# Optimization experiments

Measured on AMD Instinct MI355X. Metric: run time of the kernel, lower is better.

## Reference

```python
import jax, jax.numpy as jnp
import numpy as np

NUM_HEADS = 8
NUM_GROUPS = 32  # min(32, channels=256)
EPS = 1e-5


def group_norm(x, w, b):
    # x: [B, C, L]
    B, C, L = x.shape
    xg = x.reshape(B, NUM_GROUPS, C // NUM_GROUPS, L)
    mu = xg.mean(axis=(2, 3), keepdims=True)
    var = xg.var(axis=(2, 3), keepdims=True)
    xn = ((xg - mu) * jax.lax.rsqrt(var + EPS)).reshape(B, C, L)
    return xn * w[None, :, None] + b[None, :, None]


def setup_inputs() -> dict:
    key = jax.random.key(0)
    ks = jax.random.split(key, 5)
    B, C, L = 4, 256, 2048
    x = jax.random.normal(ks[0], (B, C, L), dtype=jnp.float32)
    gn_w = jnp.ones((C,), dtype=jnp.float32)
    gn_b = jnp.zeros((C,), dtype=jnp.float32)
    qkv_w = jax.random.normal(ks[1], (3 * C, C), dtype=jnp.float32) * (C ** -0.5)
    qkv_b = jax.random.normal(ks[2], (3 * C,), dtype=jnp.float32) * 0.02
    out_w = jax.random.normal(ks[3], (C, C), dtype=jnp.float32) * (C ** -0.5)
    out_b = jax.random.normal(ks[4], (C,), dtype=jnp.float32) * 0.02
    return {"x": x, "gn_w": gn_w, "gn_b": gn_b, "qkv_w": qkv_w,
            "qkv_b": qkv_b, "out_w": out_w, "out_b": out_b}


def reference(x, gn_w, gn_b, qkv_w, qkv_b, out_w, out_b):
    B, C, L = x.shape
    H = NUM_HEADS
    D = C // H
    h = group_norm(x, gn_w, gn_b)
    # 1x1 conv == channel matmul: [B,3C,L]
    qkv = jnp.einsum('oc,bcl->bol', qkv_w, h) + qkv_b[None, :, None]
    qkv = qkv.reshape(B, 3, H, D, L)
    q, k, v = qkv[:, 0], qkv[:, 1], qkv[:, 2]  # each [B,H,D,L]
    scale = D ** -0.5
    attn = jnp.einsum('bhdn,bhdm->bhnm', q * scale, k)  # [B,H,L,L]
    attn = jax.nn.softmax(attn, axis=-1)
    h = jnp.einsum('bhnm,bhdm->bhdn', attn, v).reshape(B, C, L)
    out = jnp.einsum('oc,bcl->bol', out_w, h) + out_b[None, :, None]
    return x + out
```

## Files before the change

### kernel.cpp

```cpp
#include <hip/hip_runtime.h>
#include <math.h>

using f32x4  = __attribute__((ext_vector_type(4))) float;
using bf16x8 = __attribute__((ext_vector_type(8))) short;

constexpr int kB = 4, kC = 256, kL = 2048, kH = 8;
constexpr float kQScale = 0.25505402264f;

__device__ __forceinline__ unsigned short f2bf(float f) {
    unsigned u = __builtin_bit_cast(unsigned, f);
    u += 0x7fffu + ((u >> 16) & 1u);
    return (unsigned short)(u >> 16);
}
__device__ __forceinline__ unsigned cvt_pk(float lo, float hi) {
    unsigned r;
    asm("v_cvt_pk_bf16_f32 %0, %1, %2" : "=v"(r) : "v"(lo), "v"(hi));
    return r;
}
__device__ __forceinline__ f32x4 mfma16(bf16x8 a, bf16x8 b, f32x4 c) {
    return __builtin_amdgcn_mfma_f32_16x16x32_bf16(a, b, c, 0, 0, 0);
}
__device__ __forceinline__ bf16x8 bc8(unsigned a, unsigned b, unsigned c, unsigned d) {
    return __builtin_bit_cast(bf16x8, make_uint4(a, b, c, d));
}
__device__ __forceinline__ void glds16(const unsigned short* g, unsigned short* l) {
    __builtin_amdgcn_global_load_lds(
        (const __attribute__((address_space(1))) unsigned int*)g,
        (__attribute__((address_space(3))) unsigned int*)l, 16, 0, 0);
}

__global__ __launch_bounds__(256) void gncvt_kernel(const float* __restrict__ x,
                                                    const float* __restrict__ gw,
                                                    const float* __restrict__ gb,
                                                    unsigned short* __restrict__ hT,
                                                    const float* __restrict__ qkvw,
                                                    const float* __restrict__ outw,
                                                    unsigned short* __restrict__ wq,
                                                    unsigned short* __restrict__ wo) {
    if (blockIdx.x >= 128) {
        int i = (blockIdx.x - 128) * 256 + threadIdx.x;
        const float* s; unsigned short* d; int j;
        if (i < 49152) { s = qkvw; d = wq; j = i; }
        else           { s = outw; d = wo; j = i - 49152; }
        float4 v = ((const float4*)s)[j];
        ((uint2*)d)[j] = make_uint2(cvt_pk(v.x, v.y), cvt_pk(v.z, v.w));
        return;
    }
    int b = blockIdx.x >> 5, g = blockIdx.x & 31;
    int t = threadIdx.x;
    const float* xp = x + ((size_t)b * kC + g * 8) * kL + 8 * t;

    float v[8][8];
    float s = 0.f, ss = 0.f;
#pragma unroll
    for (int c = 0; c < 8; ++c) {
        float4 a  = *(const float4*)(xp + (size_t)c * kL);
        float4 a2 = *(const float4*)(xp + (size_t)c * kL + 4);
        v[c][0]=a.x; v[c][1]=a.y; v[c][2]=a.z; v[c][3]=a.w;
        v[c][4]=a2.x; v[c][5]=a2.y; v[c][6]=a2.z; v[c][7]=a2.w;
        s  += (a.x+a.y)+(a.z+a.w)+(a2.x+a2.y)+(a2.z+a2.w);
        ss += a.x*a.x+a.y*a.y+a.z*a.z+a.w*a.w+a2.x*a2.x+a2.y*a2.y+a2.z*a2.z+a2.w*a2.w;
    }
#pragma unroll
    for (int off = 32; off; off >>= 1) {
        s  += __shfl_down(s, off);
        ss += __shfl_down(ss, off);
    }
    __shared__ float red[8];
    int wv = t >> 6;
    if ((t & 63) == 0) { red[wv] = s; red[4 + wv] = ss; }
    __syncthreads();
    s  = red[0] + red[1] + red[2] + red[3];
    ss = red[4] + red[5] + red[6] + red[7];
    float mean = s * (1.f / 16384.f);
    float var  = ss * (1.f / 16384.f) - mean * mean;
    float rstd = rsqrtf(var + 1e-5f);

    float wc[8], bc[8];
#pragma unroll
    for (int c = 0; c < 8; ++c) { wc[c] = gw[g*8+c] * rstd; bc[c] = gb[g*8+c]; }

    unsigned short* hp = hT + ((size_t)b * kL + 8 * t) * kC + g * 8;
#pragma unroll
    for (int j = 0; j < 8; ++j) {
        unsigned pk[4];
#pragma unroll
        for (int c2 = 0; c2 < 4; ++c2) {
            pk[c2] = cvt_pk((v[2*c2  ][j] - mean) * wc[2*c2  ] + bc[2*c2  ],
                            (v[2*c2+1][j] - mean) * wc[2*c2+1] + bc[2*c2+1]);
        }
        *(uint4*)(hp + (size_t)j * kC) = make_uint4(pk[0], pk[1], pk[2], pk[3]);
    }
}

__device__ __forceinline__ void store_qk(unsigned short* __restrict__ base, size_t bh,
                                         int n, int d0, f32x4 acc,
                                         const float* bias4, float scale) {
    float v0 = (acc[0] + bias4[0]) * scale, v1 = (acc[1] + bias4[1]) * scale;
    float v2 = (acc[2] + bias4[2]) * scale, v3 = (acc[3] + bias4[3]) * scale;
    *(uint2*)(base + (bh * kL + n) * 32 + d0) = make_uint2(cvt_pk(v0, v1), cvt_pk(v2, v3));
}

__global__ __launch_bounds__(256) void qkv_gemm(const unsigned short* __restrict__ Wb,
                                                const unsigned short* __restrict__ hT,
                                                const float* __restrict__ qkvb,
                                                unsigned short* __restrict__ qT,
                                                unsigned short* __restrict__ kT,
                                                unsigned short* __restrict__ vbuf) {
    __shared__ alignas(16) unsigned short Hlds[2][8][512];
    int t = threadIdx.x, wv = t >> 6, ll = t & 15, lg = (t >> 4) & 3;
    int lane = t & 63;
    int n0 = blockIdx.x * 128, o0 = blockIdx.y * 64, b = blockIdx.z;
    int obase = o0 + wv * 16;
    const unsigned short* hb = hT + (size_t)b * kL * kC;

    bf16x8 wf[8];
#pragma unroll
    for (int k = 0; k < 8; ++k)
        wf[k] = *(const bf16x8*)(Wb + (size_t)(obase + ll) * 256 + 32 * k + 8 * lg);
    float bias[4];
#pragma unroll
    for (int r = 0; r < 4; ++r) bias[r] = qkvb[obase + 4 * lg + r];
    int mode = (obase < 256) ? 0 : (obase < 512 ? 1 : 2);
    int d0 = (obase & 31) + 4 * lg;

    const unsigned short* hsrc0 = hb + (size_t)(n0 + 16 * (2 * wv)     + ll) * 256 + 8 * lg;
    const unsigned short* hsrc1 = hb + (size_t)(n0 + 16 * (2 * wv + 1) + ll) * 256 + 8 * lg;

    glds16(hsrc0,      &Hlds[0][2 * wv][0]);
    glds16(hsrc1,      &Hlds[0][2 * wv + 1][0]);
    glds16(hsrc0 + 32, &Hlds[1][2 * wv][0]);
    glds16(hsrc1 + 32, &Hlds[1][2 * wv + 1][0]);
    asm volatile("s_waitcnt vmcnt(2)" ::: "memory");
    __builtin_amdgcn_sched_barrier(0);
    __builtin_amdgcn_s_barrier();

    f32x4 acc[8] = {};
    int cur = 0;
    for (int c = 0; c < 8; ++c) {
        bf16x8 hf[8];
#pragma unroll
        for (int nj = 0; nj < 8; ++nj)
            hf[nj] = *(const bf16x8*)&Hlds[cur][nj][lane * 8];
        asm volatile("s_waitcnt lgkmcnt(0)" ::: "memory");
        __builtin_amdgcn_sched_barrier(0);
        __builtin_amdgcn_s_barrier();

        int kn = ((c + 2) & 7) * 32;
        glds16(hsrc0 + kn, &Hlds[cur][2 * wv][0]);
        glds16(hsrc1 + kn, &Hlds[cur][2 * wv + 1][0]);

        __builtin_amdgcn_s_setprio(1);
#pragma unroll
        for (int nj = 0; nj < 8; ++nj)
            acc[nj] = mfma16(wf[c], hf[nj], acc[nj]);
        __builtin_amdgcn_s_setprio(0);

        asm volatile("s_waitcnt vmcnt(2)" ::: "memory");
        __builtin_amdgcn_sched_barrier(0);
        __builtin_amdgcn_s_barrier();
        cur ^= 1;
    }
    asm volatile("s_waitcnt vmcnt(0)" ::: "memory");

#pragma unroll
    for (int nj = 0; nj < 8; ++nj) {
        int n = n0 + 16 * nj + ll;
        if (mode == 0) {
            store_qk(qT, (size_t)b * kH + (obase >> 5), n, d0, acc[nj], bias, kQScale);
        } else if (mode == 1) {
            store_qk(kT, (size_t)b * kH + ((obase - 256) >> 5), n, d0, acc[nj], bias, 1.f);
        } else {
#pragma unroll
            for (int r = 0; r < 4; ++r) {
                size_t row = (size_t)b * kC + (obase - 512) + 4 * lg + r;
                vbuf[row * kL + n] = f2bf(acc[nj][r] + bias[r]);
            }
        }
    }
}

__global__ __launch_bounds__(256) void attn_kernel(const unsigned short* __restrict__ qT,
                                                   const unsigned short* __restrict__ kT,
                                                   const unsigned short* __restrict__ vbuf,
                                                   unsigned short* __restrict__ h2T) {
    __shared__ alignas(16) unsigned short Klds[2][4][512];
    __shared__ alignas(16) unsigned short Vlds[2][4][512];
    __shared__ unsigned Plds[4][16][34];
    int t = threadIdx.x, wv = t >> 6, ll = t & 15, hi = (t >> 4) & 3;
    int lane = t & 63;
    int j = blockIdx.x;
    int bid = (j & 7) * 128 + (j >> 3);
    int qg = bid & 31, bh = bid >> 5;
    int b = bh >> 3, h = bh & 7;
    const unsigned short* qb = qT + (size_t)bh * kL * 32;
    const unsigned short* kb = kT + (size_t)bh * kL * 32;
    const unsigned short* vb = vbuf + ((size_t)b * kC + h * 32) * kL;
    int nq = qg * 64 + wv * 16;

    bf16x8 qf = *(const bf16x8*)(qb + (size_t)(nq + ll) * 32 + 8 * hi);

    f32x4 acc[2] = {};
    float lsum = 0.f;
    const f32x4 zero = {0.f, 0.f, 0.f, 0.f};

    const unsigned short* ksrc = kb + (size_t)(16 * wv + ll) * 32 + 8 * hi;
    const unsigned short* vsrc = vb + (size_t)(16 * (wv >> 1) + ll) * kL + 32 * (wv & 1) + 8 * hi;

    glds16(ksrc, &Klds[0][wv][0]);
    glds16(vsrc, &Vlds[0][wv][0]);
    glds16(ksrc + (size_t)64 * 32, &Klds[1][wv][0]);
    glds16(vsrc + 64,              &Vlds[1][wv][0]);
    asm volatile("s_waitcnt vmcnt(2)" ::: "memory");
    __builtin_amdgcn_sched_barrier(0);
    __builtin_amdgcn_s_barrier();

    int cur = 0;
    for (int it = 0; it < 32; ++it) {
        bf16x8 ka[4], va[2][2];
#pragma unroll
        for (int mj = 0; mj < 4; ++mj)
            ka[mj] = *(const bf16x8*)&Klds[cur][mj][lane * 8];
#pragma unroll
        for (int dj = 0; dj < 2; ++dj)
#pragma unroll
            for (int tt = 0; tt < 2; ++tt)
                va[dj][tt] = *(const bf16x8*)&Vlds[cur][dj * 2 + tt][lane * 8];

        asm volatile("s_waitcnt lgkmcnt(0)" ::: "memory");
        __builtin_amdgcn_sched_barrier(0);
        __builtin_amdgcn_s_barrier();

        int kn = ((it + 2) & 31) * 64;
        glds16(ksrc + (size_t)kn * 32, &Klds[cur][wv][0]);
        glds16(vsrc + kn,              &Vlds[cur][wv][0]);

        f32x4 s[4];
        __builtin_amdgcn_s_setprio(1);
#pragma unroll
        for (int mj = 0; mj < 4; ++mj)
            s[mj] = mfma16(ka[mj], qf, zero);
        __builtin_amdgcn_s_setprio(0);

#pragma unroll
        for (int mj = 0; mj < 4; ++mj) {
            float p0 = __builtin_amdgcn_exp2f(s[mj][0]);
            float p1 = __builtin_amdgcn_exp2f(s[mj][1]);
            float p2 = __builtin_amdgcn_exp2f(s[mj][2]);
            float p3 = __builtin_amdgcn_exp2f(s[mj][3]);
            lsum += (p0 + p1) + (p2 + p3);
            *(uint2*)&Plds[wv][ll][8 * mj + 2 * hi] =
                make_uint2(cvt_pk(p0, p1), cvt_pk(p2, p3));
        }

        bf16x8 pbf[2];
#pragma unroll
        for (int tt = 0; tt < 2; ++tt) {
            uint2 lo  = *(uint2*)&Plds[wv][ll][16 * tt + 4 * hi];
            uint2 hi2 = *(uint2*)&Plds[wv][ll][16 * tt + 4 * hi + 2];
            pbf[tt] = bc8(lo.x, lo.y, hi2.x, hi2.y);
        }

        __builtin_amdgcn_s_setprio(1);
#pragma unroll
        for (int tt = 0; tt < 2; ++tt)
#pragma unroll
            for (int dj = 0; dj < 2; ++dj)
                acc[dj] = mfma16(va[dj][tt], pbf[tt], acc[dj]);
        __builtin_amdgcn_s_setprio(0);

        asm volatile("s_waitcnt vmcnt(2)" ::: "memory");
        __builtin_amdgcn_sched_barrier(0);
        __builtin_amdgcn_s_barrier();
        cur ^= 1;
    }
    asm volatile("s_waitcnt vmcnt(0)" ::: "memory");

    lsum += __shfl_xor(lsum, 16);
    lsum += __shfl_xor(lsum, 32);
    float inv = 1.f / lsum;
    unsigned short* ob = h2T + ((size_t)b * kL + nq + ll) * kC + h * 32;
    *(uint2*)(ob + 4 * hi)      = make_uint2(cvt_pk(acc[0][0] * inv, acc[0][1] * inv),
                                             cvt_pk(acc[0][2] * inv, acc[0][3] * inv));
    *(uint2*)(ob + 16 + 4 * hi) = make_uint2(cvt_pk(acc[1][0] * inv, acc[1][1] * inv),
                                             cvt_pk(acc[1][2] * inv, acc[1][3] * inv));
}

__global__ __launch_bounds__(256) void out_gemm(const unsigned short* __restrict__ Wb,
                                                const unsigned short* __restrict__ h2T,
                                                const float* __restrict__ outb,
                                                const float* __restrict__ x,
                                                float* __restrict__ out) {
    __shared__ alignas(16) unsigned short Hlds[2][8][512];
    int t = threadIdx.x, wv = t >> 6, ll = t & 15, lg = (t >> 4) & 3;
    int lane = t & 63;
    int n0 = blockIdx.x * 128, o0 = blockIdx.y * 64, b = blockIdx.z;
    int obase = o0 + wv * 16;
    const unsigned short* hb = h2T + (size_t)b * kL * kC;

    bf16x8 wf[8];
#pragma unroll
    for (int k = 0; k < 8; ++k)
        wf[k] = *(const bf16x8*)(Wb + (size_t)(obase + ll) * 256 + 32 * k + 8 * lg);
    float bias[4];
#pragma unroll
    for (int r = 0; r < 4; ++r) bias[r] = outb[obase + 4 * lg + r];

    const unsigned short* hsrc0 = hb + (size_t)(n0 + 16 * (2 * wv)     + ll) * 256 + 8 * lg;
    const unsigned short* hsrc1 = hb + (size_t)(n0 + 16 * (2 * wv + 1) + ll) * 256 + 8 * lg;

    glds16(hsrc0,      &Hlds[0][2 * wv][0]);
    glds16(hsrc1,      &Hlds[0][2 * wv + 1][0]);
    glds16(hsrc0 + 32, &Hlds[1][2 * wv][0]);
    glds16(hsrc1 + 32, &Hlds[1][2 * wv + 1][0]);
    asm volatile("s_waitcnt vmcnt(2)" ::: "memory");
    __builtin_amdgcn_sched_barrier(0);
    __builtin_amdgcn_s_barrier();

    f32x4 acc[8] = {};
    int cur = 0;
    for (int c = 0; c < 8; ++c) {
        bf16x8 hf[8];
#pragma unroll
        for (int nj = 0; nj < 8; ++nj)
            hf[nj] = *(const bf16x8*)&Hlds[cur][nj][lane * 8];
        asm volatile("s_waitcnt lgkmcnt(0)" ::: "memory");
        __builtin_amdgcn_sched_barrier(0);
        __builtin_amdgcn_s_barrier();

        int kn = ((c + 2) & 7) * 32;
        glds16(hsrc0 + kn, &Hlds[cur][2 * wv][0]);
        glds16(hsrc1 + kn, &Hlds[cur][2 * wv + 1][0]);

        __builtin_amdgcn_s_setprio(1);
#pragma unroll
        for (int nj = 0; nj < 8; ++nj)
            acc[nj] = mfma16(wf[c], hf[nj], acc[nj]);
        __builtin_amdgcn_s_setprio(0);

        asm volatile("s_waitcnt vmcnt(2)" ::: "memory");
        __builtin_amdgcn_sched_barrier(0);
        __builtin_amdgcn_s_barrier();
        cur ^= 1;
    }
    asm volatile("s_waitcnt vmcnt(0)" ::: "memory");

#pragma unroll
    for (int nj = 0; nj < 8; ++nj) {
        int n = n0 + 16 * nj + ll;
#pragma unroll
        for (int r = 0; r < 4; ++r) {
            size_t row = (size_t)b * kC + obase + 4 * lg + r;
            out[row * kL + n] = acc[nj][r] + bias[r] + x[row * kL + n];
        }
    }
}

extern "C" void kernel_launch(void* const* d_in, const int* in_sizes, int n_in,
                              void* d_out, int out_size, void* d_ws, size_t ws_size,
                              hipStream_t stream) {
    const float* x     = (const float*)d_in[0];
    const float* gn_w  = (const float*)d_in[1];
    const float* gn_b  = (const float*)d_in[2];
    const float* qkv_w = (const float*)d_in[3];
    const float* qkv_b = (const float*)d_in[4];
    const float* out_w = (const float*)d_in[5];
    const float* out_b = (const float*)d_in[6];
    float* out = (float*)d_out;

    char* ws = (char*)d_ws;
    const size_t MB = 1024 * 1024;
    unsigned short* hT   = (unsigned short*)(ws);
    unsigned short* qT   = (unsigned short*)(ws + 4  * MB);
    unsigned short* kT   = (unsigned short*)(ws + 8  * MB);
    unsigned short* vbuf = (unsigned short*)(ws + 12 * MB);
    unsigned short* h2T  = (unsigned short*)(ws + 16 * MB);
    unsigned short* wqkv = (unsigned short*)(ws + 20 * MB);
    unsigned short* wout = (unsigned short*)(ws + 20 * MB + 512 * 1024);

    gncvt_kernel<<<dim3(384), 256, 0, stream>>>(x, gn_w, gn_b, hT, qkv_w, out_w, wqkv, wout);
    qkv_gemm<<<dim3(16, 12, kB), 256, 0, stream>>>(wqkv, hT, qkv_b, qT, kT, vbuf);
    attn_kernel<<<dim3(1024), 256, 0, stream>>>(qT, kT, vbuf, h2T);
    out_gemm<<<dim3(16, 4, kB), 256, 0, stream>>>(wout, h2T, out_b, x, out);
}
```

Before: 71.34 us.

## Load V fragments directly into registers and keep P in registers

The attention kernel no longer stages V through LDS or round-trips the softmax probabilities P through an LDS scratch buffer. Each lane now issues small global loads for its V fragments one iteration ahead into registers. The k-dimension of the P·V MFMA is permuted so that the P values produced by the QK MFMA can be packed directly as the B operand. This removes LDS writes, reads and traffic for V and P, at the cost of many more uncoalesced 8-byte global loads, more VGPRs, and vmcnt bookkeeping that must still line up with the K glds loads.

```diff
diff --git a/kernel.cpp b/kernel.cpp
--- a/kernel.cpp
+++ b/kernel.cpp
@@ -185,8 +185,6 @@
                                                    const unsigned short* __restrict__ vbuf,
                                                    unsigned short* __restrict__ h2T) {
     __shared__ alignas(16) unsigned short Klds[2][4][512];
-    __shared__ alignas(16) unsigned short Vlds[2][4][512];
-    __shared__ unsigned Plds[4][16][34];
     int t = threadIdx.x, wv = t >> 6, ll = t & 15, hi = (t >> 4) & 3;
     int lane = t & 63;
     int j = blockIdx.x;
@@ -205,27 +203,38 @@
     const f32x4 zero = {0.f, 0.f, 0.f, 0.f};
 
     const unsigned short* ksrc = kb + (size_t)(16 * wv + ll) * 32 + 8 * hi;
-    const unsigned short* vsrc = vb + (size_t)(16 * (wv >> 1) + ll) * kL + 32 * (wv & 1) + 8 * hi;
+    const int vo0 = ll * kL + 4 * hi;
+    const int vo1 = (16 + ll) * kL + 4 * hi;
 
     glds16(ksrc, &Klds[0][wv][0]);
-    glds16(vsrc, &Vlds[0][wv][0]);
     glds16(ksrc + (size_t)64 * 32, &Klds[1][wv][0]);
-    glds16(vsrc + 64,              &Vlds[1][wv][0]);
-    asm volatile("s_waitcnt vmcnt(2)" ::: "memory");
+    uint2 va[2][2][2];
+#pragma unroll
+    for (int u = 0; u < 2; ++u)
+#pragma unroll
+        for (int hf = 0; hf < 2; ++hf) {
+            va[0][u][hf] = *(const uint2*)(vb + vo0 + 32 * u + 16 * hf);
+            va[1][u][hf] = *(const uint2*)(vb + vo1 + 32 * u + 16 * hf);
+        }
+    asm volatile("s_waitcnt vmcnt(9)" ::: "memory");
     __builtin_amdgcn_sched_barrier(0);
     __builtin_amdgcn_s_barrier();
 
     int cur = 0;
     for (int it = 0; it < 32; ++it) {
-        bf16x8 ka[4], va[2][2];
+        bf16x8 ka[4];
 #pragma unroll
         for (int mj = 0; mj < 4; ++mj)
             ka[mj] = *(const bf16x8*)&Klds[cur][mj][lane * 8];
-#pragma unroll
-        for (int dj = 0; dj < 2; ++dj)
-#pragma unroll
-            for (int tt = 0; tt < 2; ++tt)
-                va[dj][tt] = *(const bf16x8*)&Vlds[cur][dj * 2 + tt][lane * 8];
+        int mn = ((it + 1) & 31) * 64;
+        uint2 nva[2][2][2];
+#pragma unroll
+        for (int u = 0; u < 2; ++u)
+#pragma unroll
+            for (int hf = 0; hf < 2; ++hf) {
+                nva[0][u][hf] = *(const uint2*)(vb + vo0 + mn + 32 * u + 16 * hf);
+                nva[1][u][hf] = *(const uint2*)(vb + vo1 + mn + 32 * u + 16 * hf);
+            }
 
         asm volatile("s_waitcnt lgkmcnt(0)" ::: "memory");
         __builtin_amdgcn_sched_barrier(0);
@@ -233,7 +242,6 @@
 
         int kn = ((it + 2) & 31) * 64;
         glds16(ksrc + (size_t)kn * 32, &Klds[cur][wv][0]);
-        glds16(vsrc + kn,              &Vlds[cur][wv][0]);
 
         f32x4 s[4];
         __builtin_amdgcn_s_setprio(1);
@@ -242,6 +250,7 @@
             s[mj] = mfma16(ka[mj], qf, zero);
         __builtin_amdgcn_s_setprio(0);
 
+        unsigned w[4][2];
 #pragma unroll
         for (int mj = 0; mj < 4; ++mj) {
             float p0 = __builtin_amdgcn_exp2f(s[mj][0]);
@@ -249,29 +258,31 @@
             float p2 = __builtin_amdgcn_exp2f(s[mj][2]);
             float p3 = __builtin_amdgcn_exp2f(s[mj][3]);
             lsum += (p0 + p1) + (p2 + p3);
-            *(uint2*)&Plds[wv][ll][8 * mj + 2 * hi] =
-                make_uint2(cvt_pk(p0, p1), cvt_pk(p2, p3));
-        }
-
-        bf16x8 pbf[2];
-#pragma unroll
-        for (int tt = 0; tt < 2; ++tt) {
-            uint2 lo  = *(uint2*)&Plds[wv][ll][16 * tt + 4 * hi];
-            uint2 hi2 = *(uint2*)&Plds[wv][ll][16 * tt + 4 * hi + 2];
-            pbf[tt] = bc8(lo.x, lo.y, hi2.x, hi2.y);
+            w[mj][0] = cvt_pk(p0, p1);
+            w[mj][1] = cvt_pk(p2, p3);
         }
 
         __builtin_amdgcn_s_setprio(1);
 #pragma unroll
-        for (int tt = 0; tt < 2; ++tt)
-#pragma unroll
-            for (int dj = 0; dj < 2; ++dj)
-                acc[dj] = mfma16(va[dj][tt], pbf[tt], acc[dj]);
+        for (int u = 0; u < 2; ++u) {
+            bf16x8 pb  = bc8(w[2*u][0], w[2*u][1], w[2*u+1][0], w[2*u+1][1]);
+            bf16x8 va0 = bc8(va[0][u][0].x, va[0][u][0].y, va[0][u][1].x, va[0][u][1].y);
+            bf16x8 va1 = bc8(va[1][u][0].x, va[1][u][0].y, va[1][u][1].x, va[1][u][1].y);
+            acc[0] = mfma16(va0, pb, acc[0]);
+            acc[1] = mfma16(va1, pb, acc[1]);
+        }
         __builtin_amdgcn_s_setprio(0);
 
-        asm volatile("s_waitcnt vmcnt(2)" ::: "memory");
-        __builtin_amdgcn_sched_barrier(0);
-        __builtin_amdgcn_s_barrier();
+        asm volatile("s_waitcnt vmcnt(9)" ::: "memory");
+        __builtin_amdgcn_sched_barrier(0);
+        __builtin_amdgcn_s_barrier();
+
+#pragma unroll
+        for (int dj = 0; dj < 2; ++dj)
+#pragma unroll
+            for (int u = 0; u < 2; ++u)
+#pragma unroll
+                for (int hf = 0; hf < 2; ++hf) va[dj][u][hf] = nva[dj][u][hf];
         cur ^= 1;
     }
     asm volatile("s_waitcnt vmcnt(0)" ::: "memory");
```

After: 165.3 us. 132% more time.
